# Performance work log

Hardware: AMD Instinct MI355X
Metric: run time of the kernel (lower is better)

Reference implementation:

```python
import jax, jax.numpy as jnp
import numpy as np

DIM = 3072
HEADS = 24
HEAD_DIM = 128
SEQ = 4096
BATCH = 1
EPS = 1e-6


def setup_inputs() -> dict:
    key = jax.random.key(0)
    ks = jax.random.split(key, 12)
    s = 1.0 / np.sqrt(DIM)
    return {
        "hidden_states": jax.random.normal(ks[0], (BATCH, SEQ, DIM), dtype=jnp.float32),
        "cos": jax.random.uniform(ks[1], (SEQ, HEAD_DIM), dtype=jnp.float32, minval=-1.0, maxval=1.0),
        "sin": jax.random.uniform(ks[2], (SEQ, HEAD_DIM), dtype=jnp.float32, minval=-1.0, maxval=1.0),
        "Wq": jax.random.normal(ks[3], (DIM, HEADS * HEAD_DIM), dtype=jnp.float32) * s,
        "bq": jax.random.normal(ks[4], (HEADS * HEAD_DIM,), dtype=jnp.float32) * 0.02,
        "Wk": jax.random.normal(ks[5], (DIM, HEADS * HEAD_DIM), dtype=jnp.float32) * s,
        "bk": jax.random.normal(ks[6], (HEADS * HEAD_DIM,), dtype=jnp.float32) * 0.02,
        "Wv": jax.random.normal(ks[7], (DIM, HEADS * HEAD_DIM), dtype=jnp.float32) * s,
        "bv": jax.random.normal(ks[8], (HEADS * HEAD_DIM,), dtype=jnp.float32) * 0.02,
        "gq": jnp.ones((HEAD_DIM,), dtype=jnp.float32),
        "gk": jnp.ones((HEAD_DIM,), dtype=jnp.float32),
    }


def _rms_norm(x, g):
    # RMSNorm over last dim (head_dim), learnable scale g
    var = jnp.mean(jnp.square(x), axis=-1, keepdims=True)
    return x * jax.lax.rsqrt(var + EPS) * g


def _apply_rope(x, cos, sin):
    # x: [B, S, H, D]; cos/sin: [S, D]. Interleaved-pair rotation (Flux style).
    xr = x.reshape(*x.shape[:-1], HEAD_DIM // 2, 2)
    x_rot = jnp.stack((-xr[..., 1], xr[..., 0]), axis=-1).reshape(x.shape)
    c = cos[None, :, None, :]
    s = sin[None, :, None, :]
    return x * c + x_rot * s


def reference(hidden_states, cos, sin, Wq, bq, Wk, bk, Wv, bv, gq, gk):
    B, S, _ = hidden_states.shape
    q = (hidden_states @ Wq + bq).reshape(B, S, HEADS, HEAD_DIM)
    k = (hidden_states @ Wk + bk).reshape(B, S, HEADS, HEAD_DIM)
    v = (hidden_states @ Wv + bv).reshape(B, S, HEADS, HEAD_DIM)
    q = _apply_rope(_rms_norm(q, gq), cos, sin)
    k = _apply_rope(_rms_norm(k, gk), cos, sin)
    scale = 1.0 / jnp.sqrt(jnp.asarray(HEAD_DIM, dtype=q.dtype))
    scores = jnp.einsum("bqhd,bkhd->bhqk", q, k) * scale  # [B, H, S, S]
    probs = jax.nn.softmax(scores, axis=-1)
    out = jnp.einsum("bhqk,bkhd->bqhd", probs, v)  # [B, S, H, D]
    return out.reshape(B, S, HEADS * HEAD_DIM)
```

## Files before the change

kernel.cpp:

```cpp
#include <hip/hip_runtime.h>
#include <hip/hip_bf16.h>
#include <stdint.h>

#define DIM 3072
#define SEQ 4096
#define NH 24
#define HD 128

typedef __hip_bfloat16 bf16;
typedef __bf16 bfv8 __attribute__((ext_vector_type(8)));
typedef float f32x4 __attribute__((ext_vector_type(4)));
typedef float f32x16 __attribute__((ext_vector_type(16)));
typedef unsigned short us4 __attribute__((ext_vector_type(4)));
typedef unsigned short us8 __attribute__((ext_vector_type(8)));

template <int N> struct ic { static constexpr int value = N; };

__device__ __forceinline__ void async16(void* lds, const void* g) {
  __builtin_amdgcn_global_load_lds((const __attribute__((address_space(1))) void*)g,
                                   (__attribute__((address_space(3))) void*)lds, 16, 0, 0);
}

__device__ __forceinline__ unsigned short f2bf(float f) {
  unsigned int u = __builtin_bit_cast(unsigned int, f);
  u += 0x7fffu + ((u >> 16) & 1u);
  return (unsigned short)(u >> 16);
}
__device__ __forceinline__ float bf2f(unsigned short b) {
  return __builtin_bit_cast(float, (unsigned int)b << 16);
}
__device__ __forceinline__ unsigned int cvtpk(float lo, float hi) {
  unsigned int r;
  asm("v_cvt_pk_bf16_f32 %0, %1, %2" : "=v"(r) : "v"(lo), "v"(hi));
  return r;
}
__device__ __forceinline__ void pl32swap(unsigned int& a, unsigned int& b) {
  asm volatile("v_permlane32_swap_b32 %0, %1" : "+v"(a), "+v"(b));
}
#if __has_builtin(__builtin_amdgcn_exp2f)
__device__ __forceinline__ float fexp2(float x) { return __builtin_amdgcn_exp2f(x); }
#else
__device__ __forceinline__ float fexp2(float x) { return exp2f(x); }
#endif

#define MFMA16(a, b, c) __builtin_amdgcn_mfma_f32_16x16x32_bf16((a), (b), (c), 0, 0, 0)
#define MFMA32(a, b, c) __builtin_amdgcn_mfma_f32_32x32x16_bf16((a), (b), (c), 0, 0, 0)

__global__ __launch_bounds__(256) void k_prep(const float* __restrict__ hs,
    us4* __restrict__ hsb, const float* __restrict__ W0, const float* __restrict__ W1,
    const float* __restrict__ W2, unsigned short* __restrict__ T0,
    unsigned short* __restrict__ T1, unsigned short* __restrict__ T2) {
  int z = blockIdx.z;
  int t = threadIdx.x;
  if (z == 3) {
    const int n4 = SEQ * DIM / 4;
    const int stride = 48 * 48 * 256;
    const float4* in = (const float4*)hs;
    for (int i = (blockIdx.y * 48 + blockIdx.x) * 256 + t; i < n4; i += stride) {
      float4 v = in[i];
      us4 r;
      r.x = f2bf(v.x); r.y = f2bf(v.y); r.z = f2bf(v.z); r.w = f2bf(v.w);
      hsb[i] = r;
    }
    return;
  }
  const float* W = (z == 0) ? W0 : (z == 1) ? W1 : W2;
  unsigned short* T = (z == 0) ? T0 : (z == 1) ? T1 : T2;
  int kb = blockIdx.y * 64;
  int nb = blockIdx.x * 64;
  __shared__ float tile[64 * 64];
#pragma unroll
  for (int p = 0; p < 4; ++p) {
    int cid = p * 256 + t;
    int row = cid >> 4, c4 = cid & 15;
    int slot = (c4 + (row >> 3)) & 15;
    float4 v = *(const float4*)&W[(size_t)(kb + row) * DIM + nb + c4 * 4];
    *(float4*)&tile[row * 64 + slot * 4] = v;
  }
  __syncthreads();
#pragma unroll
  for (int p = 0; p < 2; ++p) {
    int cid = p * 256 + t;
    int nl = cid >> 3, c8 = cid & 7;
    us8 o;
#pragma unroll
    for (int j = 0; j < 8; ++j) {
      int k = c8 * 8 + j;
      int slot = ((nl >> 2) + (k >> 3)) & 15;
      o[j] = f2bf(tile[k * 64 + slot * 4 + (nl & 3)]);
    }
    *(us8*)&T[(size_t)(nb + nl) * DIM + kb + c8 * 8] = o;
  }
}

__global__ __launch_bounds__(256, 3) void k_gemm(const unsigned short* __restrict__ A,
    const unsigned short* __restrict__ B0, const unsigned short* __restrict__ B1,
    const unsigned short* __restrict__ B2, const float* __restrict__ c0,
    const float* __restrict__ c1, const float* __restrict__ c2,
    const float* __restrict__ cosT, const float* __restrict__ sinT,
    const float* __restrict__ gq, const float* __restrict__ gk,
    unsigned short* __restrict__ o0, unsigned short* __restrict__ o1,
    unsigned short* __restrict__ o2) {
  const int b = blockIdx.x;
  const int yb = b % 32;
  const int r2b = b / 32;
  const int xb = r2b % 24;
  const int z = r2b / 24;
  const unsigned short* Bt = (z == 0) ? B0 : (z == 1) ? B1 : B2;
  const float* bias = (z == 0) ? c0 : (z == 1) ? c1 : c2;
  unsigned short* outp = (z == 0) ? o0 : (z == 1) ? o1 : o2;
  const int nb = xb * 128;
  const int mb = yb * 128;
  const int t = threadIdx.x;
  const int w = t >> 6, l = t & 63;
  const int wr = w >> 1, wc = w & 1;
  const int lq = l & 15, lg = l >> 4;
  __shared__ unsigned short lA[128 * 64];
  __shared__ unsigned short lB[128 * 64];
  __shared__ float lds_sq[128 * 2];
  f32x4 acc[4][4];
#pragma unroll
  for (int i = 0; i < 4; ++i)
#pragma unroll
    for (int j = 0; j < 4; ++j) acc[i][j] = (f32x4){0.f, 0.f, 0.f, 0.f};

  for (int kb = 0; kb < DIM; kb += 64) {
    __syncthreads();
#pragma unroll
    for (int r = 0; r < 4; ++r) {
      int row = (w * 4 + r) * 8 + (l >> 3);
      int sl = (l & 7) ^ (row & 7);
      async16(&lA[(w * 4 + r) * 512], A + (size_t)(mb + row) * DIM + kb + sl * 8);
      async16(&lB[(w * 4 + r) * 512], Bt + (size_t)(nb + row) * DIM + kb + sl * 8);
    }
    __syncthreads();
#pragma unroll
    for (int kc = 0; kc < 2; ++kc) {
      bfv8 af[4], bfv[4];
#pragma unroll
      for (int mf = 0; mf < 4; ++mf) {
        int row = wr * 64 + mf * 16 + lq;
        af[mf] = *(const bfv8*)&lA[row * 64 + (((kc * 4 + lg) ^ (row & 7)) * 8)];
      }
#pragma unroll
      for (int nf = 0; nf < 4; ++nf) {
        int row = wc * 64 + nf * 16 + lq;
        bfv[nf] = *(const bfv8*)&lB[row * 64 + (((kc * 4 + lg) ^ (row & 7)) * 8)];
      }
#pragma unroll
      for (int mf = 0; mf < 4; ++mf)
#pragma unroll
        for (int nf = 0; nf < 4; ++nf)
          acc[mf][nf] = MFMA16(af[mf], bfv[nf], acc[mf][nf]);
    }
  }

  float bv4[4];
#pragma unroll
  for (int nf = 0; nf < 4; ++nf) bv4[nf] = bias[nb + wc * 64 + nf * 16 + lq];
#pragma unroll
  for (int mf = 0; mf < 4; ++mf)
#pragma unroll
    for (int nf = 0; nf < 4; ++nf)
#pragma unroll
      for (int r = 0; r < 4; ++r) acc[mf][nf][r] += bv4[nf];

  const int hh = nb >> 7;

  if (z == 2) {
    unsigned short* vbase = outp + (size_t)hh * HD * SEQ;
#pragma unroll
    for (int nf = 0; nf < 4; ++nf) {
      int dd = wc * 64 + nf * 16 + lq;
#pragma unroll
      for (int mf = 0; mf < 4; ++mf) {
        int s0 = mb + wr * 64 + mf * 16 + lg * 4;
        us4 pk;
#pragma unroll
        for (int r = 0; r < 4; ++r) pk[r] = f2bf(acc[mf][nf][r]);
        *(us4*)&vbase[(size_t)dd * SEQ + s0] = pk;
      }
    }
    return;
  }

  unsigned short* obase0 = outp + (size_t)hh * SEQ * HD;

  float psum[4][4];
#pragma unroll
  for (int mf = 0; mf < 4; ++mf)
#pragma unroll
    for (int r = 0; r < 4; ++r) {
      float p = acc[mf][0][r] * acc[mf][0][r];
      p += acc[mf][1][r] * acc[mf][1][r];
      p += acc[mf][2][r] * acc[mf][2][r];
      p += acc[mf][3][r] * acc[mf][3][r];
      p += __shfl_xor(p, 1);
      p += __shfl_xor(p, 2);
      p += __shfl_xor(p, 4);
      p += __shfl_xor(p, 8);
      psum[mf][r] = p;
    }
  if (lq == 0) {
#pragma unroll
    for (int mf = 0; mf < 4; ++mf)
#pragma unroll
      for (int r = 0; r < 4; ++r)
        lds_sq[(wr * 64 + mf * 16 + lg * 4 + r) * 2 + wc] = psum[mf][r];
  }
  __syncthreads();

  const float* g = (z == 0) ? gq : gk;
  float gvec[4];
#pragma unroll
  for (int nf = 0; nf < 4; ++nf) gvec[nf] = g[wc * 64 + nf * 16 + lq];
  const float qs = (z == 0) ? 0.1275174373f : 1.0f;

#pragma unroll
  for (int mf = 0; mf < 4; ++mf)
#pragma unroll
    for (int r = 0; r < 4; ++r) {
      int row = wr * 64 + mf * 16 + lg * 4 + r;
      float tot = lds_sq[row * 2] + lds_sq[row * 2 + 1];
      float rrv = rsqrtf(tot * (1.0f / 128.0f) + 1e-6f);
      int s = mb + row;
#pragma unroll
      for (int nf = 0; nf < 4; ++nf) {
        int dd = wc * 64 + nf * 16 + lq;
        float y = acc[mf][nf][r] * rrv * gvec[nf];
        float yp = __shfl_xor(y, 1);
        float cc = cosT[s * HD + dd], sn = sinT[s * HD + dd];
        float o = (lq & 1) ? fmaf(yp, sn, y * cc) : fmaf(-yp, sn, y * cc);
        obase0[(size_t)s * HD + dd] = f2bf(o * qs);
      }
    }
}

__global__ __launch_bounds__(256, 2) void k_attn(const unsigned short* __restrict__ qg,
    const unsigned short* __restrict__ kg, const unsigned short* __restrict__ vtg,
    float* __restrict__ outp) {
  const int bflat = blockIdx.x;
  const int h = bflat % 24;
  const int qb0 = (bflat / 24) * 128;
  const int t = threadIdx.x;
  const int w = t >> 6, l = t & 63;
  const int l31 = l & 31, hi = l >> 5;

  __shared__ unsigned short lKf[2 * 8192];
  __shared__ unsigned short lVf[2 * 8192];

  bfv8 qf[8];
  {
    const unsigned short* qrow = qg + ((size_t)h * SEQ + qb0 + w * 32 + l31) * HD + hi * 8;
#pragma unroll
    for (int ks = 0; ks < 8; ++ks) qf[ks] = *(const bfv8*)(qrow + ks * 16);
  }

  int kidx[8], vidx[4][2];
#pragma unroll
  for (int ks = 0; ks < 8; ++ks)
    kidx[ks] = l31 * 128 + (((ks * 2 + hi) ^ (l31 & 7) ^ ((l31 >> 3) & 1)) * 8);
#pragma unroll
  for (int dt = 0; dt < 4; ++dt)
#pragma unroll
    for (int ksub = 0; ksub < 2; ++ksub)
      vidx[dt][ksub] =
          (dt * 32 + l31) * 32 + (((ksub * 2 + hi) ^ (l31 & 3) ^ ((l31 >> 2) & 3)) * 8);

  const unsigned short *kp0, *kp1, *vp0, *vp1;
  {
    int kr0 = w * 4 + (l >> 4), kr1 = 16 + kr0;
    kp0 = kg + ((size_t)h * SEQ + kr0) * HD + (((l & 15) ^ (kr0 & 7) ^ ((kr0 >> 3) & 1)) * 8);
    kp1 = kg + ((size_t)h * SEQ + kr1) * HD + (((l & 15) ^ (kr1 & 7) ^ ((kr1 >> 3) & 1)) * 8);
    int vr0 = w * 16 + (l >> 2), vr1 = 64 + vr0;
    vp0 = vtg + ((size_t)h * HD + vr0) * SEQ + (((l & 3) ^ (vr0 & 3) ^ ((vr0 >> 2) & 3)) * 8);
    vp1 = vtg + ((size_t)h * HD + vr1) * SEQ + (((l & 3) ^ (vr1 & 3) ^ ((vr1 >> 2) & 3)) * 8);
  }

#define STAGE(B)                                                              \
  do {                                                                        \
    async16(&lKf[(B) * 8192 + w * 512], kp0);                                 \
    async16(&lKf[(B) * 8192 + 2048 + w * 512], kp1);                          \
    async16(&lKf[(B) * 8192 + 4096 + w * 512], kp0 + 32 * HD);                \
    async16(&lKf[(B) * 8192 + 6144 + w * 512], kp1 + 32 * HD);                \
    async16(&lVf[(B) * 8192 + w * 512], vp0);                                 \
    async16(&lVf[(B) * 8192 + 2048 + w * 512], vp1);                          \
    async16(&lVf[(B) * 8192 + 4096 + w * 512], vp0 + 32);                     \
    async16(&lVf[(B) * 8192 + 6144 + w * 512], vp1 + 32);                     \
    kp0 += 64 * HD; kp1 += 64 * HD; vp0 += 64; vp1 += 64;                     \
  } while (0)

  f32x16 oacc[4];
#pragma unroll
  for (int dt = 0; dt < 4; ++dt)
#pragma unroll
    for (int r = 0; r < 16; ++r) oacc[dt][r] = 0.f;
  float l_run = 0.f;

  STAGE(0);

  auto phase = [&](auto bufc, auto stagec) {
    constexpr int CUR = decltype(bufc)::value;
    constexpr int DOSTAGE = decltype(stagec)::value;
    asm volatile("s_waitcnt vmcnt(0)" ::: "memory");
    __builtin_amdgcn_s_barrier();
    __builtin_amdgcn_sched_barrier(0);
    if constexpr (DOSTAGE) STAGE(CUR ^ 1);
    __builtin_amdgcn_sched_barrier(0);

    f32x16 sa, sb;
#pragma unroll
    for (int r = 0; r < 16; ++r) { sa[r] = 0.f; sb[r] = 0.f; }
    __builtin_amdgcn_s_setprio(1);
#pragma unroll
    for (int ks = 0; ks < 8; ++ks) {
      bfv8 kfa = *(const bfv8*)&lKf[CUR * 8192 + kidx[ks]];
      bfv8 kfb = *(const bfv8*)&lKf[CUR * 8192 + 4096 + kidx[ks]];
      sa = MFMA32(kfa, qf[ks], sa);
      sb = MFMA32(kfb, qf[ks], sb);
    }
    __builtin_amdgcn_s_setprio(0);

#pragma unroll
    for (int r = 0; r < 16; ++r) { sa[r] = fexp2(sa[r]); sb[r] = fexp2(sb[r]); }
    {
      float a0 = (sa[0] + sa[1]) + (sa[2] + sa[3]);
      float a1 = (sa[4] + sa[5]) + (sa[6] + sa[7]);
      float a2 = (sa[8] + sa[9]) + (sa[10] + sa[11]);
      float a3 = (sa[12] + sa[13]) + (sa[14] + sa[15]);
      float b0 = (sb[0] + sb[1]) + (sb[2] + sb[3]);
      float b1 = (sb[4] + sb[5]) + (sb[6] + sb[7]);
      float b2 = (sb[8] + sb[9]) + (sb[10] + sb[11]);
      float b3 = (sb[12] + sb[13]) + (sb[14] + sb[15]);
      l_run += ((a0 + a1) + (a2 + a3)) + ((b0 + b1) + (b2 + b3));
    }

    bfv8 paA[2], paB[2];
    {
      unsigned int a0 = cvtpk(sa[0], sa[1]), a1 = cvtpk(sa[2], sa[3]);
      unsigned int b0 = cvtpk(sa[4], sa[5]), b1 = cvtpk(sa[6], sa[7]);
      unsigned int c0 = cvtpk(sa[8], sa[9]), c1 = cvtpk(sa[10], sa[11]);
      unsigned int d0 = cvtpk(sa[12], sa[13]), d1 = cvtpk(sa[14], sa[15]);
      pl32swap(a0, b0); pl32swap(a1, b1); pl32swap(c0, d0); pl32swap(c1, d1);
      paA[0] = __builtin_bit_cast(bfv8, make_uint4(a0, a1, b0, b1));
      paA[1] = __builtin_bit_cast(bfv8, make_uint4(c0, c1, d0, d1));
      a0 = cvtpk(sb[0], sb[1]); a1 = cvtpk(sb[2], sb[3]);
      b0 = cvtpk(sb[4], sb[5]); b1 = cvtpk(sb[6], sb[7]);
      c0 = cvtpk(sb[8], sb[9]); c1 = cvtpk(sb[10], sb[11]);
      d0 = cvtpk(sb[12], sb[13]); d1 = cvtpk(sb[14], sb[15]);
      pl32swap(a0, b0); pl32swap(a1, b1); pl32swap(c0, d0); pl32swap(c1, d1);
      paB[0] = __builtin_bit_cast(bfv8, make_uint4(a0, a1, b0, b1));
      paB[1] = __builtin_bit_cast(bfv8, make_uint4(c0, c1, d0, d1));
    }

    __builtin_amdgcn_s_setprio(1);
#pragma unroll
    for (int dt = 0; dt < 4; ++dt) {
#pragma unroll
      for (int ksub = 0; ksub < 2; ++ksub) {
        bfv8 vfa = *(const bfv8*)&lVf[CUR * 8192 + vidx[dt][ksub]];
        oacc[dt] = MFMA32(paA[ksub], vfa, oacc[dt]);
      }
#pragma unroll
      for (int ksub = 0; ksub < 2; ++ksub) {
        bfv8 vfb = *(const bfv8*)&lVf[CUR * 8192 + 4096 + vidx[dt][ksub]];
        oacc[dt] = MFMA32(paB[ksub], vfb, oacc[dt]);
      }
    }
    __builtin_amdgcn_s_setprio(0);
  };

  for (int it = 0; it < 31; ++it) {
    phase(ic<0>{}, ic<1>{});
    phase(ic<1>{}, ic<1>{});
  }
  phase(ic<0>{}, ic<1>{});
  phase(ic<1>{}, ic<0>{});

  l_run += __shfl_xor(l_run, 32);
  float linv = 1.0f / l_run;
#pragma unroll
  for (int r = 0; r < 16; ++r) {
    int qr = (r & 3) + 8 * (r >> 2) + 4 * hi;
    float lr = __shfl(linv, qr);
    float* orow = outp + (size_t)(qb0 + w * 32 + qr) * DIM + h * HD;
#pragma unroll
    for (int dt = 0; dt < 4; ++dt) orow[dt * 32 + l31] = oacc[dt][r] * lr;
  }
#undef STAGE
}

extern "C" void kernel_launch(void* const* d_in, const int* in_sizes, int n_in,
                              void* d_out, int out_size, void* d_ws, size_t ws_size,
                              hipStream_t stream) {
  const float* hs = (const float*)d_in[0];
  const float* cosT = (const float*)d_in[1];
  const float* sinT = (const float*)d_in[2];
  const float* Wq = (const float*)d_in[3];
  const float* bq = (const float*)d_in[4];
  const float* Wk = (const float*)d_in[5];
  const float* bk = (const float*)d_in[6];
  const float* Wv = (const float*)d_in[7];
  const float* bv = (const float*)d_in[8];
  const float* gq = (const float*)d_in[9];
  const float* gk = (const float*)d_in[10];
  float* out = (float*)d_out;

  char* ws = (char*)d_ws;
  const size_t SZ_HS = (size_t)SEQ * DIM * 2;
  const size_t SZ_W = (size_t)DIM * DIM * 2;
  const size_t SZ_HEAD = (size_t)NH * SEQ * HD * 2;
  unsigned short* hsb = (unsigned short*)ws;               ws += SZ_HS;
  unsigned short* WqT = (unsigned short*)ws;               ws += SZ_W;
  unsigned short* WkT = (unsigned short*)ws;               ws += SZ_W;
  unsigned short* WvT = (unsigned short*)ws;               ws += SZ_W;
  unsigned short* q_b = (unsigned short*)ws;               ws += SZ_HEAD;
  unsigned short* k_b = (unsigned short*)ws;               ws += SZ_HEAD;
  unsigned short* vtr = (unsigned short*)ws;               ws += SZ_HEAD;

  k_prep<<<dim3(48, 48, 4), dim3(256), 0, stream>>>(hs, (us4*)hsb, Wq, Wk, Wv,
                                                    WqT, WkT, WvT);
  k_gemm<<<dim3(2304), dim3(256), 0, stream>>>(hsb, WqT, WkT, WvT, bq, bk, bv,
                                               cosT, sinT, gq, gk, q_b, k_b, vtr);
  k_attn<<<dim3(768), dim3(256), 0, stream>>>(q_b, k_b, vtr, out);
}
```

Measured before the change: 508.5 us.

## Replace double-buffered async LDS loads with register-staged single-buffer prefetch in attention

Drops the double-buffered global_load_lds pipeline in the attention kernel. K/V tiles are now prefetched into registers while the current tile is computed, then written to a single LDS buffer between two barriers. This halves LDS use and raises launch bounds to 3 blocks per CU to allow more occupancy. The cost is extra VGPRs for the staging registers, two barriers per iteration, and a serialized LDS write that can no longer overlap compute.

```diff
diff --git a/kernel.cpp b/kernel.cpp
--- a/kernel.cpp
+++ b/kernel.cpp
@@ -236,7 +236,7 @@
     }
 }
 
-__global__ __launch_bounds__(256, 2) void k_attn(const unsigned short* __restrict__ qg,
+__global__ __launch_bounds__(256, 3) void k_attn(const unsigned short* __restrict__ qg,
     const unsigned short* __restrict__ kg, const unsigned short* __restrict__ vtg,
     float* __restrict__ outp) {
   const int bflat = blockIdx.x;
@@ -246,8 +246,8 @@
   const int w = t >> 6, l = t & 63;
   const int l31 = l & 31, hi = l >> 5;
 
-  __shared__ unsigned short lKf[2 * 8192];
-  __shared__ unsigned short lVf[2 * 8192];
+  __shared__ unsigned short lK[8192];
+  __shared__ unsigned short lV[8192];
 
   bfv8 qf[8];
   {
@@ -269,26 +269,38 @@
 
   const unsigned short *kp0, *kp1, *vp0, *vp1;
   {
-    int kr0 = w * 4 + (l >> 4), kr1 = 16 + kr0;
-    kp0 = kg + ((size_t)h * SEQ + kr0) * HD + (((l & 15) ^ (kr0 & 7) ^ ((kr0 >> 3) & 1)) * 8);
-    kp1 = kg + ((size_t)h * SEQ + kr1) * HD + (((l & 15) ^ (kr1 & 7) ^ ((kr1 >> 3) & 1)) * 8);
-    int vr0 = w * 16 + (l >> 2), vr1 = 64 + vr0;
-    vp0 = vtg + ((size_t)h * HD + vr0) * SEQ + (((l & 3) ^ (vr0 & 3) ^ ((vr0 >> 2) & 3)) * 8);
-    vp1 = vtg + ((size_t)h * HD + vr1) * SEQ + (((l & 3) ^ (vr1 & 3) ^ ((vr1 >> 2) & 3)) * 8);
-  }
-
-#define STAGE(B)                                                              \
+    int kr0_ = w * 4 + (l >> 4), kr1_ = 16 + kr0_;
+    kp0 = kg + ((size_t)h * SEQ + kr0_) * HD + (((l & 15) ^ (kr0_ & 7) ^ ((kr0_ >> 3) & 1)) * 8);
+    kp1 = kg + ((size_t)h * SEQ + kr1_) * HD + (((l & 15) ^ (kr1_ & 7) ^ ((kr1_ >> 3) & 1)) * 8);
+    int vr0_ = w * 16 + (l >> 2), vr1_ = 64 + vr0_;
+    vp0 = vtg + ((size_t)h * HD + vr0_) * SEQ + (((l & 3) ^ (vr0_ & 3) ^ ((vr0_ >> 2) & 3)) * 8);
+    vp1 = vtg + ((size_t)h * HD + vr1_) * SEQ + (((l & 3) ^ (vr1_ & 3) ^ ((vr1_ >> 2) & 3)) * 8);
+  }
+
+  uint4 krg[4], vrg[4];
+#define LOADPAIR()                                                            \
   do {                                                                        \
-    async16(&lKf[(B) * 8192 + w * 512], kp0);                                 \
-    async16(&lKf[(B) * 8192 + 2048 + w * 512], kp1);                          \
-    async16(&lKf[(B) * 8192 + 4096 + w * 512], kp0 + 32 * HD);                \
-    async16(&lKf[(B) * 8192 + 6144 + w * 512], kp1 + 32 * HD);                \
-    async16(&lVf[(B) * 8192 + w * 512], vp0);                                 \
-    async16(&lVf[(B) * 8192 + 2048 + w * 512], vp1);                          \
-    async16(&lVf[(B) * 8192 + 4096 + w * 512], vp0 + 32);                     \
-    async16(&lVf[(B) * 8192 + 6144 + w * 512], vp1 + 32);                     \
+    krg[0] = *(const uint4*)kp0;                                              \
+    krg[1] = *(const uint4*)kp1;                                              \
+    krg[2] = *(const uint4*)(kp0 + 32 * HD);                                  \
+    krg[3] = *(const uint4*)(kp1 + 32 * HD);                                  \
+    vrg[0] = *(const uint4*)vp0;                                              \
+    vrg[1] = *(const uint4*)vp1;                                              \
+    vrg[2] = *(const uint4*)(vp0 + 32);                                       \
+    vrg[3] = *(const uint4*)(vp1 + 32);                                       \
     kp0 += 64 * HD; kp1 += 64 * HD; vp0 += 64; vp1 += 64;                     \
   } while (0)
+#define WRITEPAIR()                                                           \
+  do {                                                                        \
+    *(uint4*)&lK[w * 512 + l * 8] = krg[0];                                   \
+    *(uint4*)&lK[2048 + w * 512 + l * 8] = krg[1];                            \
+    *(uint4*)&lK[4096 + w * 512 + l * 8] = krg[2];                            \
+    *(uint4*)&lK[6144 + w * 512 + l * 8] = krg[3];                            \
+    *(uint4*)&lV[w * 512 + l * 8] = vrg[0];                                   \
+    *(uint4*)&lV[2048 + w * 512 + l * 8] = vrg[1];                            \
+    *(uint4*)&lV[4096 + w * 512 + l * 8] = vrg[2];                            \
+    *(uint4*)&lV[6144 + w * 512 + l * 8] = vrg[3];                            \
+  } while (0)
 
   f32x16 oacc[4];
 #pragma unroll
@@ -297,16 +309,13 @@
     for (int r = 0; r < 16; ++r) oacc[dt][r] = 0.f;
   float l_run = 0.f;
 
-  STAGE(0);
-
-  auto phase = [&](auto bufc, auto stagec) {
-    constexpr int CUR = decltype(bufc)::value;
-    constexpr int DOSTAGE = decltype(stagec)::value;
-    asm volatile("s_waitcnt vmcnt(0)" ::: "memory");
-    __builtin_amdgcn_s_barrier();
-    __builtin_amdgcn_sched_barrier(0);
-    if constexpr (DOSTAGE) STAGE(CUR ^ 1);
-    __builtin_amdgcn_sched_barrier(0);
+  LOADPAIR();
+  __syncthreads();
+  WRITEPAIR();
+  __syncthreads();
+
+  for (int tt = 0; tt < 64; ++tt) {
+    if (tt < 63) LOADPAIR();
 
     f32x16 sa, sb;
 #pragma unroll
@@ -314,8 +323,8 @@
     __builtin_amdgcn_s_setprio(1);
 #pragma unroll
     for (int ks = 0; ks < 8; ++ks) {
-      bfv8 kfa = *(const bfv8*)&lKf[CUR * 8192 + kidx[ks]];
-      bfv8 kfb = *(const bfv8*)&lKf[CUR * 8192 + 4096 + kidx[ks]];
+      bfv8 kfa = *(const bfv8*)&lK[kidx[ks]];
+      bfv8 kfb = *(const bfv8*)&lK[4096 + kidx[ks]];
       sa = MFMA32(kfa, qf[ks], sa);
       sb = MFMA32(kfb, qf[ks], sb);
     }
@@ -358,24 +367,23 @@
     for (int dt = 0; dt < 4; ++dt) {
 #pragma unroll
       for (int ksub = 0; ksub < 2; ++ksub) {
-        bfv8 vfa = *(const bfv8*)&lVf[CUR * 8192 + vidx[dt][ksub]];
+        bfv8 vfa = *(const bfv8*)&lV[vidx[dt][ksub]];
         oacc[dt] = MFMA32(paA[ksub], vfa, oacc[dt]);
       }
 #pragma unroll
       for (int ksub = 0; ksub < 2; ++ksub) {
-        bfv8 vfb = *(const bfv8*)&lVf[CUR * 8192 + 4096 + vidx[dt][ksub]];
+        bfv8 vfb = *(const bfv8*)&lV[4096 + vidx[dt][ksub]];
         oacc[dt] = MFMA32(paB[ksub], vfb, oacc[dt]);
       }
     }
     __builtin_amdgcn_s_setprio(0);
-  };
-
-  for (int it = 0; it < 31; ++it) {
-    phase(ic<0>{}, ic<1>{});
-    phase(ic<1>{}, ic<1>{});
-  }
-  phase(ic<0>{}, ic<1>{});
-  phase(ic<1>{}, ic<0>{});
+
+    if (tt < 63) {
+      __syncthreads();
+      WRITEPAIR();
+      __syncthreads();
+    }
+  }
 
   l_run += __shfl_xor(l_run, 32);
   float linv = 1.0f / l_run;
@@ -387,7 +395,8 @@
 #pragma unroll
     for (int dt = 0; dt < 4; ++dt) orow[dt * 32 + l31] = oacc[dt][r] * lr;
   }
-#undef STAGE
+#undef LOADPAIR
+#undef WRITEPAIR
 }
 
 extern "C" void kernel_launch(void* const* d_in, const int* in_sizes, int n_in,
```

New measurement: 757.0 us. 1.49x slower.
